# Kernel tuning notes

Measured on AMD Instinct MI355X. Metric: run time of the kernel, lower is better.

Reference implementation:

```python
import jax, jax.numpy as jnp
import numpy as np
import math

# SS2D (VMamba v2) config
D_MODEL = 96
D_INNER = 192          # ssm_ratio * d_model (== d_expand, ssm_rank_ratio==ssm_ratio)
D_STATE = 16
DT_RANK = 6            # ceil(96/16)
K = 4                  # scan directions
D_CONV = 3
STEP = 2               # EfficientScan step_size
BATCH, H, W = 4, 64, 64  # H,W chosen even -> no padding branch
LN_EPS = 1e-5


def efficient_scan(x):
    # x: (B, C, H, W) with H,W divisible by STEP -> (B, 4, C, (H/2)*(W/2))
    Bn, C = x.shape[0], x.shape[1]
    xt = jnp.swapaxes(x, 2, 3)  # (B, C, W, H)
    xs0 = x[:, :, ::STEP, ::STEP].reshape(Bn, C, -1)
    xs1 = xt[:, :, ::STEP, 1::STEP].reshape(Bn, C, -1)
    xs2 = x[:, :, ::STEP, 1::STEP].reshape(Bn, C, -1)
    xs3 = xt[:, :, 1::STEP, 1::STEP].reshape(Bn, C, -1)
    return jnp.stack([xs0, xs1, xs2, xs3], axis=1)


def efficient_merge(ys, ori_h, ori_w):
    # ys: (B, 4, C, L') -> (B, C, ori_h*ori_w)
    Bn, _, C, _ = ys.shape
    Hs, Ws = ori_h // STEP, ori_w // STEP
    a = ys[:, 0].reshape(Bn, C, Hs, Ws)
    b = jnp.swapaxes(ys[:, 1].reshape(Bn, C, Ws, Hs), 2, 3)
    c = ys[:, 2].reshape(Bn, C, Hs, Ws)
    d = jnp.swapaxes(ys[:, 3].reshape(Bn, C, Ws, Hs), 2, 3)
    y = jnp.zeros((Bn, C, ori_h, ori_w), ys.dtype)
    y = y.at[:, :, ::STEP, ::STEP].set(a)
    y = y.at[:, :, 1::STEP, ::STEP].set(b)
    y = y.at[:, :, ::STEP, 1::STEP].set(c)
    y = y.at[:, :, 1::STEP, 1::STEP].set(d)
    return y.reshape(Bn, C, ori_h * ori_w)


def selective_scan(u, delta, A, Bs, Cs, D, delta_bias):
    # u, delta: (B, K*Dg, L); A: (K*Dg, N); Bs, Cs: (B, K, N, L); D, delta_bias: (K*Dg,)
    Bn, KD, L = u.shape
    N = A.shape[1]
    Dg = KD // K
    delta = jax.nn.softplus(delta + delta_bias[None, :, None])
    u4 = u.reshape(Bn, K, Dg, L)
    dt4 = delta.reshape(Bn, K, Dg, L)
    A4 = A.reshape(K, Dg, N)
    # discretized transition / input, time-major for scan: (L, B, K, Dg, N)
    dA = jnp.exp(jnp.einsum('bkdl,kdn->lbkdn', dt4, A4))
    dBu = jnp.einsum('bkdl,bknl,bkdl->lbkdn', dt4, Bs, u4)

    def step(h, inp):
        dA_t, dBu_t = inp
        h = dA_t * h + dBu_t
        return h, h

    h0 = jnp.zeros((Bn, K, Dg, N), u.dtype)
    _, hs = jax.lax.scan(step, h0, (dA, dBu))  # (L, B, K, Dg, N)
    y = jnp.einsum('lbkdn,bknl->bkdl', hs, Cs)
    y = y + u4 * D.reshape(1, K, Dg, 1)
    return y.reshape(Bn, KD, L)


def setup_inputs() -> dict:
    key = jax.random.key(0)
    ks = jax.random.split(key, 10)
    f = jnp.float32
    x = jax.random.normal(ks[0], (BATCH, H, W, D_MODEL), f)
    W_in = jax.random.normal(ks[1], (2 * D_INNER, D_MODEL), f) / math.sqrt(D_MODEL)
    conv_w = jax.random.normal(ks[2], (D_INNER, 1, D_CONV, D_CONV), f) / math.sqrt(D_CONV * D_CONV)
    conv_b = jax.random.normal(ks[3], (D_INNER,), f) * 0.01
    x_proj_weight = jax.random.normal(ks[4], (K, DT_RANK + 2 * D_STATE, D_INNER), f) / math.sqrt(D_INNER)
    dt_projs_weight = jax.random.normal(ks[5], (K, D_INNER, DT_RANK), f) / math.sqrt(DT_RANK)
    dt_projs_bias = jax.random.normal(ks[6], (K, D_INNER), f) * 0.1
    A_logs = jnp.log(jnp.tile(jnp.arange(1, D_STATE + 1, dtype=f), (K * D_INNER, 1)))
    Ds = jnp.ones((K * D_INNER,), f)
    ln_g = jnp.ones((D_INNER,), f)
    ln_b = jnp.zeros((D_INNER,), f)
    W_out = jax.random.normal(ks[7], (D_MODEL, D_INNER), f) / math.sqrt(D_INNER)
    return dict(x=x, W_in=W_in, conv_w=conv_w, conv_b=conv_b,
                x_proj_weight=x_proj_weight, dt_projs_weight=dt_projs_weight,
                dt_projs_bias=dt_projs_bias, A_logs=A_logs, Ds=Ds,
                ln_g=ln_g, ln_b=ln_b, W_out=W_out)


def _ss2d_forward(x, W_in, conv_w, conv_b, x_proj_weight, dt_projs_weight,
                  dt_projs_bias, A_logs, Ds, ln_g, ln_b, W_out):
    Bn = x.shape[0]
    # in_proj (no bias), split into x and gate z
    xz = jnp.einsum('bhwc,ec->bhwe', x, W_in)            # (B,H,W,2*D_INNER)
    xin, z = jnp.split(xz, 2, axis=-1)
    z = jax.nn.silu(z)
    # depthwise conv 3x3 (SAME) + SiLU, NCHW
    xc = jnp.transpose(xin, (0, 3, 1, 2))                 # (B, D_INNER, H, W)
    xc = jax.lax.conv_general_dilated(
        xc, conv_w, window_strides=(1, 1), padding=((1, 1), (1, 1)),
        feature_group_count=D_INNER,
        dimension_numbers=('NCHW', 'OIHW', 'NCHW')) + conv_b[None, :, None, None]
    xc = jax.nn.silu(xc)
    # cross_selective_scan
    xs = efficient_scan(xc)                               # (B, 4, C, L')
    Lp = xs.shape[-1]
    x_dbl = jnp.einsum('bkdl,kcd->bkcl', xs, x_proj_weight)
    dts, Bs, Cs = jnp.split(x_dbl, [DT_RANK, DT_RANK + D_STATE], axis=2)
    dts = jnp.einsum('bkrl,kdr->bkdl', dts, dt_projs_weight)
    u = xs.reshape(Bn, -1, Lp).astype(jnp.float32)
    delta = dts.reshape(Bn, -1, Lp).astype(jnp.float32)
    A = -jnp.exp(A_logs.astype(jnp.float32))
    ys = selective_scan(u, delta, A, Bs.astype(jnp.float32), Cs.astype(jnp.float32),
                        Ds.astype(jnp.float32), dt_projs_bias.reshape(-1).astype(jnp.float32))
    ys = ys.reshape(Bn, K, -1, Lp)
    y = efficient_merge(ys, H, W)                         # (B, C, H*W)
    y = jnp.swapaxes(y, 1, 2)                             # (B, L, C)
    # LayerNorm over channel dim
    mu = jnp.mean(y, axis=-1, keepdims=True)
    var = jnp.var(y, axis=-1, keepdims=True)
    y = (y - mu) * jax.lax.rsqrt(var + LN_EPS) * ln_g + ln_b
    y = y.reshape(Bn, H, W, D_INNER).astype(x.dtype)
    # gate and out_proj (no bias)
    y = y * z
    out = jnp.einsum('bhwd,od->bhwo', y, W_out)
    return out


def reference(x, W_in, conv_w, conv_b, x_proj_weight, dt_projs_weight,
              dt_projs_bias, A_logs, Ds, ln_g, ln_b, W_out):
    return _ss2d_forward(x, W_in, conv_w, conv_b, x_proj_weight, dt_projs_weight,
                         dt_projs_bias, A_logs, Ds, ln_g, ln_b, W_out)
```

## Files before the change

kernel.cpp:

```cpp
#include <hip/hip_runtime.h>
#include <math.h>


#define DINNER 192
#define NSTATE 16
#define KDIR 4
#define BATCH 4
#define NPIX (BATCH * 64 * 64)
#define LP 1024
#define NCH 64
#define CHUNK 16
#define NBK (BATCH * KDIR)
#define NSTATES (NBK * DINNER * NSTATE)
#define SSTRIDE (NBK * DINNER)
#define USTRIDE 196
#define GSTRIDE 200

typedef __attribute__((ext_vector_type(8))) short short8;
typedef __attribute__((ext_vector_type(4))) short short4v;
typedef __attribute__((ext_vector_type(4))) float f32x4;

__device__ __forceinline__ float silu_f(float x) {
    return x / (1.0f + __expf(-x));
}
__device__ __forceinline__ float softplus_f(float a) {
    return (a > 20.0f) ? a : __logf(1.0f + __expf(a));
}
__device__ __forceinline__ unsigned short f2bf(float f) {
    unsigned u = __float_as_uint(f);
    unsigned r = (u + 0x7FFFu + ((u >> 16) & 1u)) >> 16;
    return (unsigned short)r;
}
__device__ __forceinline__ float bf2f(unsigned short h) {
    return __uint_as_float(((unsigned)h) << 16);
}

__global__ __launch_bounds__(256) void k_cast(
        const float* __restrict__ x, const float* __restrict__ W_in,
        const float* __restrict__ W_out,
        unsigned short* __restrict__ x_hi, unsigned short* __restrict__ x_lo,
        unsigned short* __restrict__ Wi_hi, unsigned short* __restrict__ Wi_lo,
        unsigned short* __restrict__ Wo_bf) {
    int i = blockIdx.x * 256 + threadIdx.x;
    if (i < NPIX * 96) {
        float v = x[i];
        unsigned short h = f2bf(v);
        x_hi[i] = h;
        x_lo[i] = f2bf(v - bf2f(h));
    }
    if (i < 384 * 96) {
        float v = W_in[i];
        unsigned short h = f2bf(v);
        Wi_hi[i] = h;
        Wi_lo[i] = f2bf(v - bf2f(h));
    }
    if (i < 96 * DINNER) Wo_bf[i] = f2bf(W_out[i]);
}

__global__ __launch_bounds__(256) void k_inproj3(
        const unsigned short* __restrict__ x_hi,
        const unsigned short* __restrict__ x_lo,
        const unsigned short* __restrict__ Wi_hi,
        const unsigned short* __restrict__ Wi_lo,
        float* __restrict__ xin, float* __restrict__ z) {
    int p0 = blockIdx.x * 16;
    int w = threadIdx.x >> 6;
    int lane = threadIdx.x & 63;
    int m = lane & 15, quad = lane >> 4;
    const short* xh = (const short*)x_hi;
    const short* xl = (const short*)x_lo;
    const short* wh = (const short*)Wi_hi;
    const short* wl = (const short*)Wi_lo;
    short8 ah[3], al[3];
    #pragma unroll
    for (int c = 0; c < 3; ++c) {
        size_t o = (size_t)(p0 + m) * 96 + c * 32 + quad * 8;
        ah[c] = *(const short8*)(xh + o);
        al[c] = *(const short8*)(xl + o);
    }
    #pragma unroll
    for (int i = 0; i < 6; ++i) {
        int e0 = (w * 6 + i) * 16;
        f32x4 acc = {0.f, 0.f, 0.f, 0.f};
        #pragma unroll
        for (int c = 0; c < 3; ++c) {
            size_t o = (size_t)(e0 + m) * 96 + c * 32 + quad * 8;
            short8 bh = *(const short8*)(wh + o);
            short8 bl = *(const short8*)(wl + o);
            acc = __builtin_amdgcn_mfma_f32_16x16x32_bf16(ah[c], bl, acc, 0, 0, 0);
            acc = __builtin_amdgcn_mfma_f32_16x16x32_bf16(al[c], bh, acc, 0, 0, 0);
            acc = __builtin_amdgcn_mfma_f32_16x16x32_bf16(ah[c], bh, acc, 0, 0, 0);
        }
        int e = e0 + m;
        #pragma unroll
        for (int r = 0; r < 4; ++r) {
            int p = p0 + quad * 4 + r;
            if (e < 192) xin[(size_t)p * 192 + e] = acc[r];
            else         z[(size_t)p * 192 + (e - 192)] = silu_f(acc[r]);
        }
    }
}

__global__ __launch_bounds__(192) void k_conv8(
        const float* __restrict__ xin, const float* __restrict__ cw,
        const float* __restrict__ cb, float* __restrict__ xg) {
    int blk = blockIdx.x;
    int b = blk >> 9;
    int rem = blk & 511;
    int h = rem >> 3;
    int w0 = (rem & 7) * 8;
    int d = threadIdx.x;
    float wr[3][3];
    #pragma unroll
    for (int i = 0; i < 3; ++i)
        #pragma unroll
        for (int j = 0; j < 3; ++j) wr[i][j] = cw[d * 9 + i * 3 + j];
    float bias = cb[d];
    float acc[8];
    #pragma unroll
    for (int o = 0; o < 8; ++o) acc[o] = bias;
    #pragma unroll
    for (int jj = 0; jj < 10; ++jj) {
        int ww = w0 + jj - 1;
        float r0 = 0.0f, r1 = 0.0f, r2 = 0.0f;
        if ((unsigned)ww < 64u) {
            const float* base = xin + ((size_t)b * 4096 + h * 64 + ww) * 192 + d;
            if (h > 0)  r0 = base[-64 * 192];
            r1 = base[0];
            if (h < 63) r2 = base[64 * 192];
        }
        #pragma unroll
        for (int dd2 = 0; dd2 < 3; ++dd2) {
            int o = jj - 2 + dd2;
            int cj = 2 - dd2;
            if (o >= 0 && o < 8) {
                acc[o] = fmaf(r0, wr[0][cj], acc[o]);
                acc[o] = fmaf(r1, wr[1][cj], acc[o]);
                acc[o] = fmaf(r2, wr[2][cj], acc[o]);
            }
        }
    }
    #pragma unroll
    for (int o = 0; o < 8; ++o) {
        int w = w0 + o;
        int kq = (h & 1) ? ((w & 1) ? 3 : 1) : ((w & 1) ? 2 : 0);
        int l = (kq & 1) ? ((w >> 1) * 32 + (h >> 1))
                         : ((h >> 1) * 32 + (w >> 1));
        xg[((size_t)(b * 4 + kq) * 1024 + l) * 192 + d] = silu_f(acc[o]);
    }
}

__global__ __launch_bounds__(192) void k_scan1g(
        const float* __restrict__ xg, const float* __restrict__ xpw,
        const float* __restrict__ A_logs, const float* __restrict__ dtw,
        const float* __restrict__ dtb,
        float* __restrict__ Sbuf, float* __restrict__ Qbuf) {
    __shared__ float sU[CHUNK * USTRIDE];
    __shared__ float sB[CHUNK * 16];
    __shared__ float sR[CHUNK * 8];
    int bk = blockIdx.x >> 6;
    int ch = blockIdx.x & 63;
    int k = bk & 3;
    int t = threadIdx.x;
    int d = t;
    int lbase = bk * 1024 + ch * CHUNK;
    const float4* usrc = (const float4*)(xg + (size_t)lbase * 192);
    for (int i = t; i < CHUNK * 48; i += 192) {
        int l = i / 48, c4 = i - l * 48;
        *(float4*)&sU[l * USTRIDE + c4 * 4] = usrc[i];
    }
    float A[16];
    #pragma unroll
    for (int n = 0; n < 16; ++n) A[n] = -__expf(A_logs[(k * 192 + d) * 16 + n]);
    float A0 = A[0];
    bool geo = true;
    #pragma unroll
    for (int n = 1; n < 16; ++n)
        geo = geo && (fabsf(A[n] - (float)(n + 1) * A0) <= 1e-4f * fabsf(A[n]));
    float wp[6];
    #pragma unroll
    for (int q = 0; q < 6; ++q) wp[q] = dtw[(k * 192 + d) * 6 + q];
    float bias = dtb[k * 192 + d];
    __syncthreads();
    {
        int l = t & 15, cgp = t >> 4;
        float acc0 = 0.0f, acc1 = 0.0f;
        const float* wb = xpw + (size_t)k * 38 * 192;
        int c1 = cgp + 12;
        int c1r = (c1 < 22) ? c1 : cgp;
        for (int qv = 0; qv < 48; ++qv) {
            float4 xv = *(const float4*)&sU[l * USTRIDE + qv * 4];
            float4 w0 = *(const float4*)&wb[(size_t)cgp * 192 + qv * 4];
            float4 w1 = *(const float4*)&wb[(size_t)c1r * 192 + qv * 4];
            acc0 = fmaf(xv.x, w0.x, fmaf(xv.y, w0.y, fmaf(xv.z, w0.z, fmaf(xv.w, w0.w, acc0))));
            acc1 = fmaf(xv.x, w1.x, fmaf(xv.y, w1.y, fmaf(xv.z, w1.z, fmaf(xv.w, w1.w, acc1))));
        }
        if (cgp < 6) sR[l * 8 + cgp] = acc0;
        else         sB[l * 16 + (cgp - 6)] = acc0;
        if (c1 < 22) sB[l * 16 + (c1 - 6)] = acc1;
    }
    __syncthreads();
    float h[16];
    #pragma unroll
    for (int n = 0; n < 16; ++n) h[n] = 0.0f;
    float S = 0.0f;
    for (int l = 0; l < CHUNK; ++l) {
        float a = bias;
        #pragma unroll
        for (int q = 0; q < 6; ++q) a = fmaf(wp[q], sR[l * 8 + q], a);
        float dlt = softplus_f(a);
        S += dlt;
        float du = dlt * sU[l * USTRIDE + d];
        if (geo) {
            float e1 = __expf(dlt * A0);
            float e = e1;
            #pragma unroll
            for (int n = 0; n < 16; ++n) {
                h[n] = fmaf(e, h[n], du * sB[l * 16 + n]);
                e *= e1;
            }
        } else {
            #pragma unroll
            for (int n = 0; n < 16; ++n) {
                float e = __expf(dlt * A[n]);
                h[n] = fmaf(e, h[n], du * sB[l * 16 + n]);
            }
        }
    }
    Sbuf[(size_t)ch * SSTRIDE + bk * 192 + d] = S;
    size_t base = (size_t)ch * NSTATES + bk * (192 * 16);
    #pragma unroll
    for (int n = 0; n < 16; ++n)
        Qbuf[base + n * 192 + d] = h[n];
}

__global__ __launch_bounds__(256) void k_scan2(
        const float* __restrict__ Sbuf, const float* __restrict__ A_logs,
        float* QH) {
    int s = blockIdx.x * 256 + threadIdx.x;
    int bk = s / 3072;
    int rem = s - bk * 3072;
    int n = rem / 192;
    int d = rem - n * 192;
    int k = bk & 3;
    float A = -__expf(A_logs[(k * 192 + d) * 16 + n]);
    float h = 0.0f;
    for (int c = 0; c < NCH; ++c) {
        float q = QH[(size_t)c * NSTATES + s];
        float S = Sbuf[(size_t)c * SSTRIDE + bk * 192 + d];
        float p = __expf(A * S);
        QH[(size_t)c * NSTATES + s] = h;
        h = fmaf(p, h, q);
    }
}

__global__ __launch_bounds__(192) void k_scan3g(
        const float* __restrict__ xg, const float* __restrict__ xpw,
        const float* __restrict__ A_logs, const float* __restrict__ dtw,
        const float* __restrict__ dtb, const float* __restrict__ Ds,
        const float* __restrict__ QH, float* __restrict__ yout) {
    __shared__ float sU[CHUNK * USTRIDE];
    __shared__ float sB[CHUNK * 16];
    __shared__ float sC[CHUNK * 16];
    __shared__ float sR[CHUNK * 8];
    int bk = blockIdx.x >> 6;
    int ch = blockIdx.x & 63;
    int k = bk & 3;
    int t = threadIdx.x;
    int d = t;
    int lbase = bk * 1024 + ch * CHUNK;
    const float4* usrc = (const float4*)(xg + (size_t)lbase * 192);
    for (int i = t; i < CHUNK * 48; i += 192) {
        int l = i / 48, c4 = i - l * 48;
        *(float4*)&sU[l * USTRIDE + c4 * 4] = usrc[i];
    }
    float A[16];
    #pragma unroll
    for (int n = 0; n < 16; ++n) A[n] = -__expf(A_logs[(k * 192 + d) * 16 + n]);
    float A0 = A[0];
    bool geo = true;
    #pragma unroll
    for (int n = 1; n < 16; ++n)
        geo = geo && (fabsf(A[n] - (float)(n + 1) * A0) <= 1e-4f * fabsf(A[n]));
    float wp[6];
    #pragma unroll
    for (int q = 0; q < 6; ++q) wp[q] = dtw[(k * 192 + d) * 6 + q];
    float bias = dtb[k * 192 + d];
    float Dp = Ds[k * 192 + d];
    __syncthreads();
    {
        int l = t & 15, cgp = t >> 4;
        float acc[4] = {0.f, 0.f, 0.f, 0.f};
        int c3 = (cgp < 2) ? (cgp + 36) : cgp;
        const float* wb = xpw + (size_t)k * 38 * 192;
        for (int qv = 0; qv < 48; ++qv) {
            float4 xv = *(const float4*)&sU[l * USTRIDE + qv * 4];
            float4 w0 = *(const float4*)&wb[(cgp +  0) * 192 + qv * 4];
            float4 w1 = *(const float4*)&wb[(cgp + 12) * 192 + qv * 4];
            float4 w2 = *(const float4*)&wb[(cgp + 24) * 192 + qv * 4];
            float4 w3 = *(const float4*)&wb[(size_t)c3 * 192 + qv * 4];
            acc[0] = fmaf(xv.x, w0.x, fmaf(xv.y, w0.y, fmaf(xv.z, w0.z, fmaf(xv.w, w0.w, acc[0]))));
            acc[1] = fmaf(xv.x, w1.x, fmaf(xv.y, w1.y, fmaf(xv.z, w1.z, fmaf(xv.w, w1.w, acc[1]))));
            acc[2] = fmaf(xv.x, w2.x, fmaf(xv.y, w2.y, fmaf(xv.z, w2.z, fmaf(xv.w, w2.w, acc[2]))));
            acc[3] = fmaf(xv.x, w3.x, fmaf(xv.y, w3.y, fmaf(xv.z, w3.z, fmaf(xv.w, w3.w, acc[3]))));
        }
        #pragma unroll
        for (int j = 0; j < 4; ++j) {
            int c = cgp + 12 * j;
            if (j == 3) { if (cgp >= 2) break; c = cgp + 36; }
            float v = acc[j];
            if (c < 6)       sR[l * 8 + c] = v;
            else if (c < 22) sB[l * 16 + (c - 6)] = v;
            else             sC[l * 16 + (c - 22)] = v;
        }
    }
    float h[16];
    size_t base = (size_t)ch * NSTATES + bk * (192 * 16);
    #pragma unroll
    for (int n = 0; n < 16; ++n) h[n] = QH[base + n * 192 + d];
    __syncthreads();
    for (int l = 0; l < CHUNK; ++l) {
        float a = bias;
        #pragma unroll
        for (int q = 0; q < 6; ++q) a = fmaf(wp[q], sR[l * 8 + q], a);
        float dlt = softplus_f(a);
        float u = sU[l * USTRIDE + d];
        float du = dlt * u;
        float y = 0.0f;
        if (geo) {
            float e1 = __expf(dlt * A0);
            float e = e1;
            #pragma unroll
            for (int n = 0; n < 16; ++n) {
                h[n] = fmaf(e, h[n], du * sB[l * 16 + n]);
                y = fmaf(h[n], sC[l * 16 + n], y);
                e *= e1;
            }
        } else {
            #pragma unroll
            for (int n = 0; n < 16; ++n) {
                float e = __expf(dlt * A[n]);
                h[n] = fmaf(e, h[n], du * sB[l * 16 + n]);
                y = fmaf(h[n], sC[l * 16 + n], y);
            }
        }
        yout[(size_t)(lbase + l) * 192 + d] = fmaf(u, Dp, y);
    }
}

__global__ __launch_bounds__(256) void k_lnout(
        const float* __restrict__ yout, const float* __restrict__ z,
        const float* __restrict__ lng, const float* __restrict__ lnb,
        const unsigned short* __restrict__ Wo_bf, float* __restrict__ out) {
    __shared__ __align__(16) short sgb[32 * GSTRIDE];
    int p0 = blockIdx.x * 32;
    int t = threadIdx.x;
    int p = t >> 3;
    int sub = t & 7;
    int gp = p0 + p;
    int b = gp >> 12;
    int hw = gp & 4095;
    int h = hw >> 6, w = hw & 63;
    int kq = (h & 1) ? ((w & 1) ? 3 : 1) : ((w & 1) ? 2 : 0);
    int l = (kq & 1) ? ((w >> 1) * 32 + (h >> 1))
                     : ((h >> 1) * 32 + (w >> 1));
    const float* yrow = yout + ((size_t)(b * 4 + kq) * 1024 + l) * 192 + sub * 24;
    float4 yv[6];
    float s = 0.0f, s2 = 0.0f;
    #pragma unroll
    for (int j = 0; j < 6; ++j) {
        float4 v = *(const float4*)(yrow + j * 4);
        yv[j] = v;
        s += v.x + v.y + v.z + v.w;
        s2 += v.x * v.x + v.y * v.y + v.z * v.z + v.w * v.w;
    }
    #pragma unroll
    for (int off = 1; off < 8; off <<= 1) {
        s  += __shfl_xor(s, off, 8);
        s2 += __shfl_xor(s2, off, 8);
    }
    float mu = s * (1.0f / 192.0f);
    float var = s2 * (1.0f / 192.0f) - mu * mu;
    float rstd = rsqrtf(var + 1e-5f);
    const float* zrow = z + (size_t)gp * 192 + sub * 24;
    short* grow = sgb + p * GSTRIDE + sub * 24;
    #pragma unroll
    for (int j = 0; j < 6; ++j) {
        float4 zv = *(const float4*)(zrow + j * 4);
        float4 gv = *(const float4*)(lng + sub * 24 + j * 4);
        float4 bv = *(const float4*)(lnb + sub * 24 + j * 4);
        short4v sv;
        sv.x = (short)f2bf(((yv[j].x - mu) * rstd * gv.x + bv.x) * zv.x);
        sv.y = (short)f2bf(((yv[j].y - mu) * rstd * gv.y + bv.y) * zv.y);
        sv.z = (short)f2bf(((yv[j].z - mu) * rstd * gv.z + bv.z) * zv.z);
        sv.w = (short)f2bf(((yv[j].w - mu) * rstd * gv.w + bv.w) * zv.w);
        *(short4v*)(grow + j * 4) = sv;
    }
    __syncthreads();
    int wv = t >> 6;
    int lane = t & 63;
    int m = lane & 15, quad = lane >> 4;
    int mt = wv >> 1;
    int nb = (wv & 1) * 3;
    const short* wob = (const short*)Wo_bf;
    short8 a[6];
    #pragma unroll
    for (int kk = 0; kk < 6; ++kk)
        a[kk] = *(const short8*)(sgb + (mt * 16 + m) * GSTRIDE + kk * 32 + quad * 8);
    #pragma unroll
    for (int i = 0; i < 3; ++i) {
        int n0 = (nb + i) * 16;
        f32x4 acc = {0.f, 0.f, 0.f, 0.f};
        #pragma unroll
        for (int kk = 0; kk < 6; ++kk) {
            short8 bfr = *(const short8*)(wob + (size_t)(n0 + m) * 192 + kk * 32 + quad * 8);
            acc = __builtin_amdgcn_mfma_f32_16x16x32_bf16(a[kk], bfr, acc, 0, 0, 0);
        }
        #pragma unroll
        for (int r = 0; r < 4; ++r) {
            int pp = p0 + mt * 16 + quad * 4 + r;
            out[(size_t)pp * 96 + n0 + m] = acc[r];
        }
    }
}

extern "C" void kernel_launch(void* const* d_in, const int* in_sizes, int n_in,
                              void* d_out, int out_size, void* d_ws, size_t ws_size,
                              hipStream_t stream) {
    const float* x    = (const float*)d_in[0];
    const float* W_in = (const float*)d_in[1];
    const float* cw   = (const float*)d_in[2];
    const float* cb   = (const float*)d_in[3];
    const float* xpw  = (const float*)d_in[4];
    const float* dtw  = (const float*)d_in[5];
    const float* dtb  = (const float*)d_in[6];
    const float* Alog = (const float*)d_in[7];
    const float* Ds   = (const float*)d_in[8];
    const float* lng  = (const float*)d_in[9];
    const float* lnb  = (const float*)d_in[10];
    const float* Wout = (const float*)d_in[11];
    float* out = (float*)d_out;

    float* ws = (float*)d_ws;
    size_t off = 0;
    unsigned short* x_hi  = (unsigned short*)(ws + off); off += NPIX * 96 / 2;
    unsigned short* x_lo  = (unsigned short*)(ws + off); off += NPIX * 96 / 2;
    unsigned short* Wi_hi = (unsigned short*)(ws + off); off += 384 * 96 / 2;
    unsigned short* Wi_lo = (unsigned short*)(ws + off); off += 384 * 96 / 2;
    unsigned short* Wo_bf = (unsigned short*)(ws + off); off += 96 * DINNER / 2;
    float* xin   = ws + off; off += (size_t)NPIX * 192;
    float* zbuf  = ws + off; off += (size_t)NPIX * 192;
    float* xg    = ws + off; off += (size_t)NPIX * 192;
    float* Sbuf  = ws + off; off += (size_t)NCH * SSTRIDE;
    float* QH    = ws + off; off += (size_t)NCH * NSTATES;
    float* yout  = ws + off; off += (size_t)NBK * LP * 192;

    hipLaunchKernelGGL(k_cast, dim3((NPIX * 96 + 255) / 256), dim3(256), 0, stream,
                       x, W_in, Wout, x_hi, x_lo, Wi_hi, Wi_lo, Wo_bf);
    hipLaunchKernelGGL(k_inproj3, dim3(NPIX / 16), dim3(256), 0, stream,
                       x_hi, x_lo, Wi_hi, Wi_lo, xin, zbuf);
    hipLaunchKernelGGL(k_conv8, dim3(NPIX / 8), dim3(192), 0, stream,
                       xin, cw, cb, xg);
    hipLaunchKernelGGL(k_scan1g, dim3(NBK * NCH), dim3(192), 0, stream,
                       xg, xpw, Alog, dtw, dtb, Sbuf, QH);
    hipLaunchKernelGGL(k_scan2, dim3(NSTATES / 256), dim3(256), 0, stream,
                       Sbuf, Alog, QH);
    hipLaunchKernelGGL(k_scan3g, dim3(NBK * NCH), dim3(192), 0, stream,
                       xg, xpw, Alog, dtw, dtb, Ds, QH, yout);
    hipLaunchKernelGGL(k_lnout, dim3(NPIX / 32), dim3(256), 0, stream,
                       yout, zbuf, lng, lnb, Wo_bf, out);
}
```

Measured before the change: 181.0 us.

## Fuse LayerNorm, gating and out-projection into scan kernel; split x inside in-proj

The hi/lo bf16 split of x now happens inside the in-projection kernel, so the separate cast pass and its x_hi/x_lo buffers are gone. The final scan stage now keeps its chunk outputs in shared memory and applies LayerNorm, z-gating and the MFMA out-projection in the same kernel, scattering rows to their merged pixel positions. This removes the yout round-trip through global memory and one kernel launch. In exchange the scan kernel uses more shared memory and does more work per block, and the zbuf reads and output writes are now scattered by pixel.

After: 186.8 us. +3.2%, slower.

```diff
diff --git a/kernel.cpp b/kernel.cpp
--- a/kernel.cpp
+++ b/kernel.cpp
@@ -17,7 +17,6 @@
 #define GSTRIDE 200
 
 typedef __attribute__((ext_vector_type(8))) short short8;
-typedef __attribute__((ext_vector_type(4))) short short4v;
 typedef __attribute__((ext_vector_type(4))) float f32x4;
 
 __device__ __forceinline__ float silu_f(float x) {
@@ -35,19 +34,11 @@
     return __uint_as_float(((unsigned)h) << 16);
 }
 
-__global__ __launch_bounds__(256) void k_cast(
-        const float* __restrict__ x, const float* __restrict__ W_in,
-        const float* __restrict__ W_out,
-        unsigned short* __restrict__ x_hi, unsigned short* __restrict__ x_lo,
+__global__ __launch_bounds__(256) void k_castW(
+        const float* __restrict__ W_in, const float* __restrict__ W_out,
         unsigned short* __restrict__ Wi_hi, unsigned short* __restrict__ Wi_lo,
         unsigned short* __restrict__ Wo_bf) {
     int i = blockIdx.x * 256 + threadIdx.x;
-    if (i < NPIX * 96) {
-        float v = x[i];
-        unsigned short h = f2bf(v);
-        x_hi[i] = h;
-        x_lo[i] = f2bf(v - bf2f(h));
-    }
     if (i < 384 * 96) {
         float v = W_in[i];
         unsigned short h = f2bf(v);
@@ -58,8 +49,7 @@
 }
 
 __global__ __launch_bounds__(256) void k_inproj3(
-        const unsigned short* __restrict__ x_hi,
-        const unsigned short* __restrict__ x_lo,
+        const float* __restrict__ x,
         const unsigned short* __restrict__ Wi_hi,
         const unsigned short* __restrict__ Wi_lo,
         float* __restrict__ xin, float* __restrict__ z) {
@@ -67,16 +57,22 @@
     int w = threadIdx.x >> 6;
     int lane = threadIdx.x & 63;
     int m = lane & 15, quad = lane >> 4;
-    const short* xh = (const short*)x_hi;
-    const short* xl = (const short*)x_lo;
     const short* wh = (const short*)Wi_hi;
     const short* wl = (const short*)Wi_lo;
     short8 ah[3], al[3];
     #pragma unroll
     for (int c = 0; c < 3; ++c) {
-        size_t o = (size_t)(p0 + m) * 96 + c * 32 + quad * 8;
-        ah[c] = *(const short8*)(xh + o);
-        al[c] = *(const short8*)(xl + o);
+        const float* xr = x + (size_t)(p0 + m) * 96 + c * 32 + quad * 8;
+        short8 hi, lo;
+        #pragma unroll
+        for (int j = 0; j < 8; ++j) {
+            float v = xr[j];
+            unsigned short hb = f2bf(v);
+            hi[j] = (short)hb;
+            lo[j] = (short)f2bf(v - bf2f(hb));
+        }
+        ah[c] = hi;
+        al[c] = lo;
     }
     #pragma unroll
     for (int i = 0; i < 6; ++i) {
@@ -254,15 +250,21 @@
     }
 }
 
-__global__ __launch_bounds__(192) void k_scan3g(
+__global__ __launch_bounds__(192) void k_scan3gl(
         const float* __restrict__ xg, const float* __restrict__ xpw,
         const float* __restrict__ A_logs, const float* __restrict__ dtw,
         const float* __restrict__ dtb, const float* __restrict__ Ds,
-        const float* __restrict__ QH, float* __restrict__ yout) {
+        const float* __restrict__ QH, const float* __restrict__ zbuf,
+        const float* __restrict__ lng, const float* __restrict__ lnb,
+        const unsigned short* __restrict__ Wo_bf, float* __restrict__ out) {
     __shared__ float sU[CHUNK * USTRIDE];
     __shared__ float sB[CHUNK * 16];
     __shared__ float sC[CHUNK * 16];
     __shared__ float sR[CHUNK * 8];
+    __shared__ float red[2][12][16];
+    __shared__ float smv[2][16];
+    __shared__ int   spix[16];
+    __shared__ __align__(16) short sA[CHUNK * GSTRIDE];
     int bk = blockIdx.x >> 6;
     int ch = blockIdx.x & 63;
     int k = bk & 3;
@@ -344,82 +346,74 @@
                 y = fmaf(h[n], sC[l * 16 + n], y);
             }
         }
-        yout[(size_t)(lbase + l) * 192 + d] = fmaf(u, Dp, y);
-    }
-}
-
-__global__ __launch_bounds__(256) void k_lnout(
-        const float* __restrict__ yout, const float* __restrict__ z,
-        const float* __restrict__ lng, const float* __restrict__ lnb,
-        const unsigned short* __restrict__ Wo_bf, float* __restrict__ out) {
-    __shared__ __align__(16) short sgb[32 * GSTRIDE];
-    int p0 = blockIdx.x * 32;
-    int t = threadIdx.x;
-    int p = t >> 3;
-    int sub = t & 7;
-    int gp = p0 + p;
-    int b = gp >> 12;
-    int hw = gp & 4095;
-    int h = hw >> 6, w = hw & 63;
-    int kq = (h & 1) ? ((w & 1) ? 3 : 1) : ((w & 1) ? 2 : 0);
-    int l = (kq & 1) ? ((w >> 1) * 32 + (h >> 1))
-                     : ((h >> 1) * 32 + (w >> 1));
-    const float* yrow = yout + ((size_t)(b * 4 + kq) * 1024 + l) * 192 + sub * 24;
-    float4 yv[6];
-    float s = 0.0f, s2 = 0.0f;
-    #pragma unroll
-    for (int j = 0; j < 6; ++j) {
-        float4 v = *(const float4*)(yrow + j * 4);
-        yv[j] = v;
-        s += v.x + v.y + v.z + v.w;
-        s2 += v.x * v.x + v.y * v.y + v.z * v.z + v.w * v.w;
-    }
-    #pragma unroll
-    for (int off = 1; off < 8; off <<= 1) {
-        s  += __shfl_xor(s, off, 8);
-        s2 += __shfl_xor(s2, off, 8);
-    }
-    float mu = s * (1.0f / 192.0f);
-    float var = s2 * (1.0f / 192.0f) - mu * mu;
-    float rstd = rsqrtf(var + 1e-5f);
-    const float* zrow = z + (size_t)gp * 192 + sub * 24;
-    short* grow = sgb + p * GSTRIDE + sub * 24;
-    #pragma unroll
-    for (int j = 0; j < 6; ++j) {
-        float4 zv = *(const float4*)(zrow + j * 4);
-        float4 gv = *(const float4*)(lng + sub * 24 + j * 4);
-        float4 bv = *(const float4*)(lnb + sub * 24 + j * 4);
-        short4v sv;
-        sv.x = (short)f2bf(((yv[j].x - mu) * rstd * gv.x + bv.x) * zv.x);
-        sv.y = (short)f2bf(((yv[j].y - mu) * rstd * gv.y + bv.y) * zv.y);
-        sv.z = (short)f2bf(((yv[j].z - mu) * rstd * gv.z + bv.z) * zv.z);
-        sv.w = (short)f2bf(((yv[j].w - mu) * rstd * gv.w + bv.w) * zv.w);
-        *(short4v*)(grow + j * 4) = sv;
-    }
-    __syncthreads();
-    int wv = t >> 6;
-    int lane = t & 63;
-    int m = lane & 15, quad = lane >> 4;
-    int mt = wv >> 1;
-    int nb = (wv & 1) * 3;
-    const short* wob = (const short*)Wo_bf;
-    short8 a[6];
-    #pragma unroll
-    for (int kk = 0; kk < 6; ++kk)
-        a[kk] = *(const short8*)(sgb + (mt * 16 + m) * GSTRIDE + kk * 32 + quad * 8);
-    #pragma unroll
-    for (int i = 0; i < 3; ++i) {
-        int n0 = (nb + i) * 16;
-        f32x4 acc = {0.f, 0.f, 0.f, 0.f};
-        #pragma unroll
-        for (int kk = 0; kk < 6; ++kk) {
-            short8 bfr = *(const short8*)(wob + (size_t)(n0 + m) * 192 + kk * 32 + quad * 8);
-            acc = __builtin_amdgcn_mfma_f32_16x16x32_bf16(a[kk], bfr, acc, 0, 0, 0);
-        }
-        #pragma unroll
-        for (int r = 0; r < 4; ++r) {
-            int pp = p0 + mt * 16 + quad * 4 + r;
-            out[(size_t)pp * 96 + n0 + m] = acc[r];
+        sU[l * USTRIDE + d] = fmaf(u, Dp, y);
+    }
+    __syncthreads();
+    {
+        int lq = t & 15, seg = t >> 4;
+        float ps = 0.0f, ps2 = 0.0f;
+        #pragma unroll
+        for (int j = 0; j < 16; ++j) {
+            float v = sU[lq * USTRIDE + seg * 16 + j];
+            ps += v;
+            ps2 += v * v;
+        }
+        red[0][seg][lq] = ps;
+        red[1][seg][lq] = ps2;
+    }
+    __syncthreads();
+    if (t < 16) {
+        float s = 0.0f, s2 = 0.0f;
+        #pragma unroll
+        for (int sg = 0; sg < 12; ++sg) { s += red[0][sg][t]; s2 += red[1][sg][t]; }
+        float mu = s * (1.0f / 192.0f);
+        float var = s2 * (1.0f / 192.0f) - mu * mu;
+        smv[0][t] = mu;
+        smv[1][t] = rsqrtf(var + 1e-5f);
+    }
+    __syncthreads();
+    {
+        float lg = lng[d], lb = lnb[d];
+        int b = bk >> 2;
+        for (int l = 0; l < CHUNK; ++l) {
+            int gl = ch * CHUNK + l;
+            int i = gl >> 5, j = gl & 31;
+            int hh, wpx;
+            if (k == 0)      { hh = 2 * i;     wpx = 2 * j;     }
+            else if (k == 1) { hh = 2 * j + 1; wpx = 2 * i;     }
+            else if (k == 2) { hh = 2 * i;     wpx = 2 * j + 1; }
+            else             { hh = 2 * j + 1; wpx = 2 * i + 1; }
+            int p = b * 4096 + hh * 64 + wpx;
+            if (d == 0) spix[l] = p;
+            float y = sU[l * USTRIDE + d];
+            float g = ((y - smv[0][l]) * smv[1][l] * lg + lb) * zbuf[(size_t)p * 192 + d];
+            sA[l * GSTRIDE + d] = (short)f2bf(g);
+        }
+    }
+    __syncthreads();
+    {
+        int wv = t >> 6;
+        int lane = t & 63;
+        int m = lane & 15, quad = lane >> 4;
+        const short* wob = (const short*)Wo_bf;
+        short8 a[6];
+        #pragma unroll
+        for (int kk = 0; kk < 6; ++kk)
+            a[kk] = *(const short8*)(sA + m * GSTRIDE + kk * 32 + quad * 8);
+        #pragma unroll
+        for (int i2 = 0; i2 < 2; ++i2) {
+            int n0 = (wv * 2 + i2) * 16;
+            f32x4 acc = {0.f, 0.f, 0.f, 0.f};
+            #pragma unroll
+            for (int kk = 0; kk < 6; ++kk) {
+                short8 bfr = *(const short8*)(wob + (size_t)(n0 + m) * 192 + kk * 32 + quad * 8);
+                acc = __builtin_amdgcn_mfma_f32_16x16x32_bf16(a[kk], bfr, acc, 0, 0, 0);
+            }
+            #pragma unroll
+            for (int r = 0; r < 4; ++r) {
+                int l = quad * 4 + r;
+                out[(size_t)spix[l] * 96 + n0 + m] = acc[r];
+            }
         }
     }
 }
@@ -443,8 +437,6 @@
 
     float* ws = (float*)d_ws;
     size_t off = 0;
-    unsigned short* x_hi  = (unsigned short*)(ws + off); off += NPIX * 96 / 2;
-    unsigned short* x_lo  = (unsigned short*)(ws + off); off += NPIX * 96 / 2;
     unsigned short* Wi_hi = (unsigned short*)(ws + off); off += 384 * 96 / 2;
     unsigned short* Wi_lo = (unsigned short*)(ws + off); off += 384 * 96 / 2;
     unsigned short* Wo_bf = (unsigned short*)(ws + off); off += 96 * DINNER / 2;
@@ -453,20 +445,18 @@
     float* xg    = ws + off; off += (size_t)NPIX * 192;
     float* Sbuf  = ws + off; off += (size_t)NCH * SSTRIDE;
     float* QH    = ws + off; off += (size_t)NCH * NSTATES;
-    float* yout  = ws + off; off += (size_t)NBK * LP * 192;
-
-    hipLaunchKernelGGL(k_cast, dim3((NPIX * 96 + 255) / 256), dim3(256), 0, stream,
-                       x, W_in, Wout, x_hi, x_lo, Wi_hi, Wi_lo, Wo_bf);
+
+    hipLaunchKernelGGL(k_castW, dim3(144), dim3(256), 0, stream,
+                       W_in, Wout, Wi_hi, Wi_lo, Wo_bf);
     hipLaunchKernelGGL(k_inproj3, dim3(NPIX / 16), dim3(256), 0, stream,
-                       x_hi, x_lo, Wi_hi, Wi_lo, xin, zbuf);
+                       x, Wi_hi, Wi_lo, xin, zbuf);
     hipLaunchKernelGGL(k_conv8, dim3(NPIX / 8), dim3(192), 0, stream,
                        xin, cw, cb, xg);
     hipLaunchKernelGGL(k_scan1g, dim3(NBK * NCH), dim3(192), 0, stream,
                        xg, xpw, Alog, dtw, dtb, Sbuf, QH);
     hipLaunchKernelGGL(k_scan2, dim3(NSTATES / 256), dim3(256), 0, stream,
                        Sbuf, Alog, QH);
-    hipLaunchKernelGGL(k_scan3g, dim3(NBK * NCH), dim3(192), 0, stream,
-                       xg, xpw, Alog, dtw, dtb, Ds, QH, yout);
-    hipLaunchKernelGGL(k_lnout, dim3(NPIX / 32), dim3(256), 0, stream,
-                       yout, zbuf, lng, lnb, Wo_bf, out);
-}
+    hipLaunchKernelGGL(k_scan3gl, dim3(NBK * NCH), dim3(192), 0, stream,
+                       xg, xpw, Alog, dtw, dtb, Ds, QH, zbuf, lng, lnb,
+                       Wo_bf, out);
+}
```

## Fuse input bf16 split into in-projection and halve scan chunk length

Applied to the files above, without the earlier changes.

The bf16 hi/lo split of x now happens inside the in-projection kernel, so the full-size cast pass and its x_hi/x_lo buffers go away. Only the weight cast remains, as a small separate kernel. The chunked scan now uses 128 chunks of 8 steps instead of 64 of 16, which doubles the block count in the scan1/scan3 kernels for more parallelism and shortens each block's serial loop. In exchange the chunk-carry pass gets twice as many sequential steps and the QH/S buffers get larger, and the per-thread x_proj projection work in both scan kernels is remapped to match.

After: 182.1 us. No clear change (+0.6%).

```diff
diff --git a/kernel.cpp b/kernel.cpp
--- a/kernel.cpp
+++ b/kernel.cpp
@@ -8,8 +8,8 @@
 #define BATCH 4
 #define NPIX (BATCH * 64 * 64)
 #define LP 1024
-#define NCH 64
-#define CHUNK 16
+#define NCH 128
+#define CHUNK 8
 #define NBK (BATCH * KDIR)
 #define NSTATES (NBK * DINNER * NSTATE)
 #define SSTRIDE (NBK * DINNER)
@@ -35,19 +35,11 @@
     return __uint_as_float(((unsigned)h) << 16);
 }
 
-__global__ __launch_bounds__(256) void k_cast(
-        const float* __restrict__ x, const float* __restrict__ W_in,
-        const float* __restrict__ W_out,
-        unsigned short* __restrict__ x_hi, unsigned short* __restrict__ x_lo,
+__global__ __launch_bounds__(256) void k_castW(
+        const float* __restrict__ W_in, const float* __restrict__ W_out,
         unsigned short* __restrict__ Wi_hi, unsigned short* __restrict__ Wi_lo,
         unsigned short* __restrict__ Wo_bf) {
     int i = blockIdx.x * 256 + threadIdx.x;
-    if (i < NPIX * 96) {
-        float v = x[i];
-        unsigned short h = f2bf(v);
-        x_hi[i] = h;
-        x_lo[i] = f2bf(v - bf2f(h));
-    }
     if (i < 384 * 96) {
         float v = W_in[i];
         unsigned short h = f2bf(v);
@@ -58,8 +50,7 @@
 }
 
 __global__ __launch_bounds__(256) void k_inproj3(
-        const unsigned short* __restrict__ x_hi,
-        const unsigned short* __restrict__ x_lo,
+        const float* __restrict__ x,
         const unsigned short* __restrict__ Wi_hi,
         const unsigned short* __restrict__ Wi_lo,
         float* __restrict__ xin, float* __restrict__ z) {
@@ -67,16 +58,22 @@
     int w = threadIdx.x >> 6;
     int lane = threadIdx.x & 63;
     int m = lane & 15, quad = lane >> 4;
-    const short* xh = (const short*)x_hi;
-    const short* xl = (const short*)x_lo;
     const short* wh = (const short*)Wi_hi;
     const short* wl = (const short*)Wi_lo;
     short8 ah[3], al[3];
     #pragma unroll
     for (int c = 0; c < 3; ++c) {
-        size_t o = (size_t)(p0 + m) * 96 + c * 32 + quad * 8;
-        ah[c] = *(const short8*)(xh + o);
-        al[c] = *(const short8*)(xl + o);
+        const float* xr = x + (size_t)(p0 + m) * 96 + c * 32 + quad * 8;
+        short8 hi, lo;
+        #pragma unroll
+        for (int j = 0; j < 8; ++j) {
+            float v = xr[j];
+            unsigned short hb = f2bf(v);
+            hi[j] = (short)hb;
+            lo[j] = (short)f2bf(v - bf2f(hb));
+        }
+        ah[c] = hi;
+        al[c] = lo;
     }
     #pragma unroll
     for (int i = 0; i < 6; ++i) {
@@ -158,8 +155,8 @@
     __shared__ float sU[CHUNK * USTRIDE];
     __shared__ float sB[CHUNK * 16];
     __shared__ float sR[CHUNK * 8];
-    int bk = blockIdx.x >> 6;
-    int ch = blockIdx.x & 63;
+    int bk = blockIdx.x >> 7;
+    int ch = blockIdx.x & 127;
     int k = bk & 3;
     int t = threadIdx.x;
     int d = t;
@@ -183,21 +180,17 @@
     float bias = dtb[k * 192 + d];
     __syncthreads();
     {
-        int l = t & 15, cgp = t >> 4;
-        float acc0 = 0.0f, acc1 = 0.0f;
+        int l = t & 7, cgp = t >> 3;
+        float acc0 = 0.0f;
         const float* wb = xpw + (size_t)k * 38 * 192;
-        int c1 = cgp + 12;
-        int c1r = (c1 < 22) ? c1 : cgp;
+        int c0 = (cgp < 22) ? cgp : 0;
         for (int qv = 0; qv < 48; ++qv) {
             float4 xv = *(const float4*)&sU[l * USTRIDE + qv * 4];
-            float4 w0 = *(const float4*)&wb[(size_t)cgp * 192 + qv * 4];
-            float4 w1 = *(const float4*)&wb[(size_t)c1r * 192 + qv * 4];
+            float4 w0 = *(const float4*)&wb[(size_t)c0 * 192 + qv * 4];
             acc0 = fmaf(xv.x, w0.x, fmaf(xv.y, w0.y, fmaf(xv.z, w0.z, fmaf(xv.w, w0.w, acc0))));
-            acc1 = fmaf(xv.x, w1.x, fmaf(xv.y, w1.y, fmaf(xv.z, w1.z, fmaf(xv.w, w1.w, acc1))));
-        }
-        if (cgp < 6) sR[l * 8 + cgp] = acc0;
-        else         sB[l * 16 + (cgp - 6)] = acc0;
-        if (c1 < 22) sB[l * 16 + (c1 - 6)] = acc1;
+        }
+        if (cgp < 6)       sR[l * 8 + cgp] = acc0;
+        else if (cgp < 22) sB[l * 16 + (cgp - 6)] = acc0;
     }
     __syncthreads();
     float h[16];
@@ -263,8 +256,8 @@
     __shared__ float sB[CHUNK * 16];
     __shared__ float sC[CHUNK * 16];
     __shared__ float sR[CHUNK * 8];
-    int bk = blockIdx.x >> 6;
-    int ch = blockIdx.x & 63;
+    int bk = blockIdx.x >> 7;
+    int ch = blockIdx.x & 127;
     int k = bk & 3;
     int t = threadIdx.x;
     int d = t;
@@ -289,30 +282,22 @@
     float Dp = Ds[k * 192 + d];
     __syncthreads();
     {
-        int l = t & 15, cgp = t >> 4;
-        float acc[4] = {0.f, 0.f, 0.f, 0.f};
-        int c3 = (cgp < 2) ? (cgp + 36) : cgp;
+        int l = t & 7, cgp = t >> 3;
+        float acc0 = 0.0f, acc1 = 0.0f;
         const float* wb = xpw + (size_t)k * 38 * 192;
+        int c1 = cgp + 24;
+        int c1r = (c1 < 38) ? c1 : cgp;
         for (int qv = 0; qv < 48; ++qv) {
             float4 xv = *(const float4*)&sU[l * USTRIDE + qv * 4];
-            float4 w0 = *(const float4*)&wb[(cgp +  0) * 192 + qv * 4];
-            float4 w1 = *(const float4*)&wb[(cgp + 12) * 192 + qv * 4];
-            float4 w2 = *(const float4*)&wb[(cgp + 24) * 192 + qv * 4];
-            float4 w3 = *(const float4*)&wb[(size_t)c3 * 192 + qv * 4];
-            acc[0] = fmaf(xv.x, w0.x, fmaf(xv.y, w0.y, fmaf(xv.z, w0.z, fmaf(xv.w, w0.w, acc[0]))));
-            acc[1] = fmaf(xv.x, w1.x, fmaf(xv.y, w1.y, fmaf(xv.z, w1.z, fmaf(xv.w, w1.w, acc[1]))));
-            acc[2] = fmaf(xv.x, w2.x, fmaf(xv.y, w2.y, fmaf(xv.z, w2.z, fmaf(xv.w, w2.w, acc[2]))));
-            acc[3] = fmaf(xv.x, w3.x, fmaf(xv.y, w3.y, fmaf(xv.z, w3.z, fmaf(xv.w, w3.w, acc[3]))));
-        }
-        #pragma unroll
-        for (int j = 0; j < 4; ++j) {
-            int c = cgp + 12 * j;
-            if (j == 3) { if (cgp >= 2) break; c = cgp + 36; }
-            float v = acc[j];
-            if (c < 6)       sR[l * 8 + c] = v;
-            else if (c < 22) sB[l * 16 + (c - 6)] = v;
-            else             sC[l * 16 + (c - 22)] = v;
-        }
+            float4 w0 = *(const float4*)&wb[(size_t)cgp * 192 + qv * 4];
+            float4 w1 = *(const float4*)&wb[(size_t)c1r * 192 + qv * 4];
+            acc0 = fmaf(xv.x, w0.x, fmaf(xv.y, w0.y, fmaf(xv.z, w0.z, fmaf(xv.w, w0.w, acc0))));
+            acc1 = fmaf(xv.x, w1.x, fmaf(xv.y, w1.y, fmaf(xv.z, w1.z, fmaf(xv.w, w1.w, acc1))));
+        }
+        if (cgp < 6)       sR[l * 8 + cgp] = acc0;
+        else if (cgp < 22) sB[l * 16 + (cgp - 6)] = acc0;
+        else               sC[l * 16 + (cgp - 22)] = acc0;
+        if (c1 < 38)       sC[l * 16 + (c1 - 22)] = acc1;
     }
     float h[16];
     size_t base = (size_t)ch * NSTATES + bk * (192 * 16);
@@ -443,8 +428,6 @@
 
     float* ws = (float*)d_ws;
     size_t off = 0;
-    unsigned short* x_hi  = (unsigned short*)(ws + off); off += NPIX * 96 / 2;
-    unsigned short* x_lo  = (unsigned short*)(ws + off); off += NPIX * 96 / 2;
     unsigned short* Wi_hi = (unsigned short*)(ws + off); off += 384 * 96 / 2;
     unsigned short* Wi_lo = (unsigned short*)(ws + off); off += 384 * 96 / 2;
     unsigned short* Wo_bf = (unsigned short*)(ws + off); off += 96 * DINNER / 2;
@@ -455,10 +438,10 @@
     float* QH    = ws + off; off += (size_t)NCH * NSTATES;
     float* yout  = ws + off; off += (size_t)NBK * LP * 192;
 
-    hipLaunchKernelGGL(k_cast, dim3((NPIX * 96 + 255) / 256), dim3(256), 0, stream,
-                       x, W_in, Wout, x_hi, x_lo, Wi_hi, Wi_lo, Wo_bf);
+    hipLaunchKernelGGL(k_castW, dim3(144), dim3(256), 0, stream,
+                       W_in, Wout, Wi_hi, Wi_lo, Wo_bf);
     hipLaunchKernelGGL(k_inproj3, dim3(NPIX / 16), dim3(256), 0, stream,
-                       x_hi, x_lo, Wi_hi, Wi_lo, xin, zbuf);
+                       x, Wi_hi, Wi_lo, xin, zbuf);
     hipLaunchKernelGGL(k_conv8, dim3(NPIX / 8), dim3(192), 0, stream,
                        xin, cw, cb, xg);
     hipLaunchKernelGGL(k_scan1g, dim3(NBK * NCH), dim3(192), 0, stream,
```
